# Kernel optimization log

Measured on AMD Instinct MI355X. Metric: run time of the kernel, lower is better.

## Reference

```python
import jax, jax.numpy as jnp
import numpy as np

B, S, H = 4, 2048, 1024
NH, HD = 8, 128  # num_heads, head_dim

def setup_inputs() -> dict:
    key = jax.random.key(0)
    ks = jax.random.split(key, 5)
    scale = 1.0 / np.sqrt(H)
    return {
        "hidden_states": jax.random.normal(ks[0], (B, S, H), dtype=jnp.float32),
        "Wq": jax.random.normal(ks[1], (H, H), dtype=jnp.float32) * scale,
        "Wk": jax.random.normal(ks[2], (H, H), dtype=jnp.float32) * scale,
        "Wv": jax.random.normal(ks[3], (H, H), dtype=jnp.float32) * scale,
        "Wo": jax.random.normal(ks[4], (H, H), dtype=jnp.float32) * scale,
    }

def reference(hidden_states, Wq, Wk, Wv, Wo):
    # projections (torch Linear: x @ W.T), weights stored [out, in]
    q = hidden_states @ Wq.T
    k = hidden_states @ Wk.T
    v = hidden_states @ Wv.T
    # [B, NH, S, HD]
    q = q.reshape(B, S, NH, HD).transpose(0, 2, 1, 3)
    k = k.reshape(B, S, NH, HD).transpose(0, 2, 1, 3)
    v = v.reshape(B, S, NH, HD).transpose(0, 2, 1, 3)
    scale = 1.0 / jnp.sqrt(jnp.asarray(HD, dtype=q.dtype))
    scores = jnp.einsum("bhqd,bhkd->bhqk", q, k) * scale
    # softmax in fp32, cast back to input dtype (matches torch F.softmax dtype=float32)
    attn = jax.nn.softmax(scores.astype(jnp.float32), axis=-1).astype(q.dtype)
    out = jnp.einsum("bhqk,bhkd->bhqd", attn, v)
    out = out.transpose(0, 2, 1, 3).reshape(B, S, H)
    return out @ Wo.T
```

## Files before the change

kernel.cpp:

```cpp
#include <hip/hip_runtime.h>
#include <stdint.h>

#define Bz  4
#define Sz  2048
#define Hz  1024
#define NHz 8
#define HDz 128
#define Mz  (Bz*Sz)

typedef __attribute__((ext_vector_type(8))) short bf16x8;
typedef __attribute__((ext_vector_type(4))) float f32x4;

__device__ __forceinline__ unsigned short f2bf(float x) {
  union { float f; unsigned int u; } c; c.f = x;
  unsigned int u = c.u;
  return (unsigned short)((u + 0x7FFFu + ((u >> 16) & 1u)) >> 16);
}

__device__ __forceinline__ void gl2lds16(const unsigned short* g, unsigned short* l) {
  __builtin_amdgcn_global_load_lds(
      (const __attribute__((address_space(1))) unsigned int*)g,
      (__attribute__((address_space(3))) unsigned int*)l, 16, 0, 0);
}

__global__ __launch_bounds__(256)
void cvt_kernel(const float* __restrict__ in, unsigned short* __restrict__ out, int n) {
  const int n4 = n >> 2;
  for (int i = blockIdx.x * blockDim.x + threadIdx.x; i < n4; i += gridDim.x * blockDim.x) {
    float4 v = ((const float4*)in)[i];
    ushort4 o;
    o.x = f2bf(v.x); o.y = f2bf(v.y); o.z = f2bf(v.z); o.w = f2bf(v.w);
    ((ushort4*)out)[i] = o;
  }
}

__global__ __launch_bounds__(256)
void cvt4_kernel(const float* __restrict__ w0, const float* __restrict__ w1,
                 const float* __restrict__ w2, const float* __restrict__ w3,
                 unsigned short* __restrict__ o0, unsigned short* __restrict__ o1,
                 unsigned short* __restrict__ o2, unsigned short* __restrict__ o3) {
  const int which = blockIdx.y;
  const float* in = (which == 0) ? w0 : (which == 1) ? w1 : (which == 2) ? w2 : w3;
  unsigned short* out = (which == 0) ? o0 : (which == 1) ? o1 : (which == 2) ? o2 : o3;
  const int n4 = (Hz * Hz) >> 2;
  for (int i = blockIdx.x * blockDim.x + threadIdx.x; i < n4; i += gridDim.x * blockDim.x) {
    float4 v = ((const float4*)in)[i];
    ushort4 o;
    o.x = f2bf(v.x); o.y = f2bf(v.y); o.z = f2bf(v.z); o.w = f2bf(v.w);
    ((ushort4*)out)[i] = o;
  }
}

#define GEMM_PROLOG()                                                           \
  __shared__ __align__(16) unsigned short Asm[128 * 64];                        \
  __shared__ __align__(16) unsigned short Bsm[128 * 64];                        \
  const int tid = threadIdx.x;                                                  \
  const int w  = tid >> 6, l = tid & 63;                                        \
  const int lc = l & 15,  lg = l >> 4;                                          \
  const int wr = w >> 1,  wc = w & 1;                                           \
  const int bm = blockIdx.x * 128;                                              \
  const int bn = blockIdx.y * 128;                                              \
  f32x4 acc[4][4];                                                              \
  _Pragma("unroll")                                                             \
  for (int i = 0; i < 4; i++)                                                   \
    _Pragma("unroll")                                                           \
    for (int j = 0; j < 4; j++) acc[i][j] = (f32x4){0.f, 0.f, 0.f, 0.f};        \
  const int srow = w * 32 + (l >> 3);                                           \
  const int scol = (l & 7) * 8;                                                 \
  for (int kt = 0; kt < 16; kt++) {                                             \
    const int k0 = kt * 64;                                                     \
    __syncthreads();                                                            \
    _Pragma("unroll")                                                           \
    for (int i = 0; i < 4; i++) {                                               \
      gl2lds16(A  + (size_t)(bm + srow + i * 8) * Hz + k0 + scol,               \
               &Asm[(w * 32 + i * 8) * 64]);                                    \
      gl2lds16(Bw + (size_t)(bn + srow + i * 8) * Hz + k0 + scol,               \
               &Bsm[(w * 32 + i * 8) * 64]);                                    \
    }                                                                           \
    __syncthreads();                                                            \
    _Pragma("unroll")                                                           \
    for (int kk = 0; kk < 2; kk++) {                                            \
      bf16x8 af[4], bf[4];                                                      \
      _Pragma("unroll")                                                         \
      for (int t = 0; t < 4; t++) {                                             \
        af[t] = *(const bf16x8*)&Asm[(wr*64 + t*16 + lc)*64 + kk*32 + lg*8];    \
        bf[t] = *(const bf16x8*)&Bsm[(wc*64 + t*16 + lc)*64 + kk*32 + lg*8];    \
      }                                                                         \
      _Pragma("unroll")                                                         \
      for (int mt = 0; mt < 4; mt++)                                            \
        _Pragma("unroll")                                                       \
        for (int nt = 0; nt < 4; nt++)                                          \
          acc[mt][nt] = __builtin_amdgcn_mfma_f32_16x16x32_bf16(                \
              af[mt], bf[nt], acc[mt][nt], 0, 0, 0);                            \
    }                                                                           \
  }

__global__ __launch_bounds__(256)
void gemm_qkv(const unsigned short* __restrict__ A,
              const unsigned short* __restrict__ W0,
              const unsigned short* __restrict__ W1,
              const unsigned short* __restrict__ W2,
              unsigned short* __restrict__ Qo,
              unsigned short* __restrict__ Ko,
              unsigned short* __restrict__ Vto, float qscale)
{
  const int z = blockIdx.z;
  const unsigned short* Bw = (z == 0) ? W0 : (z == 1) ? W1 : W2;
  const float alpha = (z == 0) ? qscale : 1.0f;
  GEMM_PROLOG()

#pragma unroll
  for (int mt = 0; mt < 4; mt++) {
#pragma unroll
    for (int nt = 0; nt < 4; nt++) {
      const int row0 = bm + wr * 64 + mt * 16 + lg * 4;
      const int col  = bn + wc * 64 + nt * 16 + lc;
      if (z == 2) {
        ushort4 pk;
        pk.x = f2bf(acc[mt][nt][0]);
        pk.y = f2bf(acc[mt][nt][1]);
        pk.z = f2bf(acc[mt][nt][2]);
        pk.w = f2bf(acc[mt][nt][3]);
        const size_t idx = ((size_t)((row0 >> 11) << 10) + col) * Sz + (row0 & 2047);
        *(ushort4*)&Vto[idx] = pk;
      } else {
        unsigned short* C = (z == 0) ? Qo : Ko;
#pragma unroll
        for (int r = 0; r < 4; r++)
          C[(size_t)(row0 + r) * Hz + col] = f2bf(acc[mt][nt][r] * alpha);
      }
    }
  }
}

__global__ __launch_bounds__(256)
void gemm_out(const unsigned short* __restrict__ A,
              const unsigned short* __restrict__ Bw,
              float* __restrict__ C)
{
  GEMM_PROLOG()
#pragma unroll
  for (int mt = 0; mt < 4; mt++)
#pragma unroll
    for (int nt = 0; nt < 4; nt++) {
      const int row0 = bm + wr * 64 + mt * 16 + lg * 4;
      const int col  = bn + wc * 64 + nt * 16 + lc;
#pragma unroll
      for (int r = 0; r < 4; r++)
        C[(size_t)(row0 + r) * Hz + col] = acc[mt][nt][r];
    }
}

__global__ __launch_bounds__(256, 2)
void attn_fwd(const unsigned short* __restrict__ Q,
              const unsigned short* __restrict__ K,
              const unsigned short* __restrict__ Vt,
              unsigned short* __restrict__ O)
{
  const int bid = blockIdx.x;
  const int wg  = (bid & 7) * 64 + (bid >> 3);
  const int qb  = wg & 15;
  const int bh  = wg >> 4;
  const int b = bh >> 3, nh = bh & 7;
  const int w = threadIdx.x >> 6, l = threadIdx.x & 63;
  const int lc = l & 15, lg = l >> 4;

  __shared__ __align__(16) unsigned short Ksm[2][64 * 128];
  __shared__ __align__(16) unsigned short Vsm[128 * 64];
  __shared__ __align__(16) unsigned short Psm[4][16 * 64];

  bf16x8 qf[2][4];
#pragma unroll
  for (int mt = 0; mt < 2; mt++)
#pragma unroll
    for (int ks = 0; ks < 4; ks++)
      qf[mt][ks] = *(const bf16x8*)(Q + ((size_t)b * Sz + qb * 128 + w * 32 + mt * 16 + lc) * Hz
                                      + nh * HDz + ks * 32 + lg * 8);

  const unsigned short* Kbase = K  + (size_t)b * Sz * Hz + nh * HDz;
  const unsigned short* Vbase = Vt + (size_t)bh * HDz * Sz;

  f32x4 acc[2][8];
#pragma unroll
  for (int mt = 0; mt < 2; mt++)
#pragma unroll
    for (int i = 0; i < 8; i++) acc[mt][i] = (f32x4){0.f, 0.f, 0.f, 0.f};
  float mrow[2][4], lrow[2][4];
#pragma unroll
  for (int mt = 0; mt < 2; mt++)
#pragma unroll
    for (int r = 0; r < 4; r++) { mrow[mt][r] = -1e30f; lrow[mt][r] = 0.f; }

  #define STAGE_K(BUF, KT) {                                                          \
    _Pragma("unroll")                                                                 \
    for (int i = 0; i < 4; i++) {                                                     \
      const int r = w * 16 + i * 4 + (l >> 4);                                        \
      gl2lds16(Kbase + (size_t)((KT) * 64 + r) * Hz + (((l & 15) ^ (r & 7)) * 8),     \
               &Ksm[BUF][(w * 16 + i * 4) * 128]);                                    \
    } }
  #define STAGE_V(KT) {                                                               \
    _Pragma("unroll")                                                                 \
    for (int i = 0; i < 4; i++) {                                                     \
      const int r = w * 32 + i * 8 + (l >> 3);                                        \
      gl2lds16(Vbase + (size_t)r * Sz + (KT) * 64 + (((l & 7) ^ (r & 7)) * 8),        \
               &Vsm[(w * 32 + i * 8) * 64]);                                          \
    } }

  int cur = 0;
  STAGE_K(0, 0);
  __syncthreads();

  for (int kt = 0; kt < Sz / 64; kt++) {
    STAGE_V(kt);
    if (kt < Sz / 64 - 1) STAGE_K(cur ^ 1, kt + 1);

    f32x4 s[2][4];
#pragma unroll
    for (int mt = 0; mt < 2; mt++)
#pragma unroll
      for (int nt = 0; nt < 4; nt++) s[mt][nt] = (f32x4){0.f, 0.f, 0.f, 0.f};
#pragma unroll
    for (int ks = 0; ks < 4; ks++) {
#pragma unroll
      for (int nt = 0; nt < 4; nt++) {
        bf16x8 kf = *(const bf16x8*)&Ksm[cur][(nt * 16 + lc) * 128 + (((ks * 4 + lg) ^ (lc & 7)) * 8)];
#pragma unroll
        for (int mt = 0; mt < 2; mt++)
          s[mt][nt] = __builtin_amdgcn_mfma_f32_16x16x32_bf16(qf[mt][ks], kf, s[mt][nt], 0, 0, 0);
      }
    }

#pragma unroll
    for (int mt = 0; mt < 2; mt++) {
#pragma unroll
      for (int r = 0; r < 4; r++) {
        float tm = fmaxf(fmaxf(s[mt][0][r], s[mt][1][r]), fmaxf(s[mt][2][r], s[mt][3][r]));
        tm = fmaxf(tm, __shfl_xor(tm, 1));
        tm = fmaxf(tm, __shfl_xor(tm, 2));
        tm = fmaxf(tm, __shfl_xor(tm, 4));
        tm = fmaxf(tm, __shfl_xor(tm, 8));
        if (tm > mrow[mt][r] + 8.0f) {
          const float sc = exp2f(mrow[mt][r] - tm);
          mrow[mt][r] = tm;
          lrow[mt][r] *= sc;
#pragma unroll
          for (int nt = 0; nt < 8; nt++) acc[mt][nt][r] *= sc;
        }
        float rs = 0.f;
#pragma unroll
        for (int nt = 0; nt < 4; nt++) {
          float p = exp2f(s[mt][nt][r] - mrow[mt][r]);
          s[mt][nt][r] = p;
          rs += p;
        }
        lrow[mt][r] += rs;
      }
    }

    bf16x8 pf[2][2];
#pragma unroll
    for (int mt = 0; mt < 2; mt++) {
#pragma unroll
      for (int nt = 0; nt < 4; nt++)
#pragma unroll
        for (int r = 0; r < 4; r++) {
          const int row = lg * 4 + r;
          const int ch  = (nt * 2 + (lc >> 3)) ^ (row & 7);
          Psm[w][row * 64 + ch * 8 + (lc & 7)] = f2bf(s[mt][nt][r]);
        }
#pragma unroll
      for (int kk = 0; kk < 2; kk++)
        pf[mt][kk] = *(const bf16x8*)&Psm[w][lc * 64 + (((kk * 4 + lg) ^ (lc & 7)) * 8)];
    }

    __syncthreads();

#pragma unroll
    for (int kk = 0; kk < 2; kk++) {
#pragma unroll
      for (int nt = 0; nt < 8; nt++) {
        bf16x8 vf = *(const bf16x8*)&Vsm[(nt * 16 + lc) * 64 + (((kk * 4 + lg) ^ (lc & 7)) * 8)];
        acc[0][nt] = __builtin_amdgcn_mfma_f32_16x16x32_bf16(pf[0][kk], vf, acc[0][nt], 0, 0, 0);
        acc[1][nt] = __builtin_amdgcn_mfma_f32_16x16x32_bf16(pf[1][kk], vf, acc[1][nt], 0, 0, 0);
      }
    }

    __syncthreads();
    cur ^= 1;
  }

#pragma unroll
  for (int mt = 0; mt < 2; mt++) {
    float inv[4];
#pragma unroll
    for (int r = 0; r < 4; r++) {
      float t = lrow[mt][r];
      t += __shfl_xor(t, 1);
      t += __shfl_xor(t, 2);
      t += __shfl_xor(t, 4);
      t += __shfl_xor(t, 8);
      inv[r] = 1.0f / t;
    }
#pragma unroll
    for (int nt = 0; nt < 8; nt++)
#pragma unroll
      for (int r = 0; r < 4; r++) {
        const size_t row = (size_t)b * Sz + qb * 128 + w * 32 + mt * 16 + lg * 4 + r;
        O[row * Hz + nh * HDz + nt * 16 + lc] = f2bf(acc[mt][nt][r] * inv[r]);
      }
  }
}

extern "C" void kernel_launch(void* const* d_in, const int* in_sizes, int n_in,
                              void* d_out, int out_size, void* d_ws, size_t ws_size,
                              hipStream_t stream) {
  const float* hs = (const float*)d_in[0];
  const float* Wq = (const float*)d_in[1];
  const float* Wk = (const float*)d_in[2];
  const float* Wv = (const float*)d_in[3];
  const float* Wo = (const float*)d_in[4];

  const size_t NEL = (size_t)Mz * Hz;
  const size_t WEL = (size_t)Hz * Hz;

  unsigned short* p = (unsigned short*)d_ws;
  unsigned short* hs_bf = p; p += NEL;
  unsigned short* Wq_bf = p; p += WEL;
  unsigned short* Wk_bf = p; p += WEL;
  unsigned short* Wv_bf = p; p += WEL;
  unsigned short* Wo_bf = p; p += WEL;
  unsigned short* Qb    = p; p += NEL;
  unsigned short* Kb    = p; p += NEL;
  unsigned short* Vtb   = p; p += NEL;
  unsigned short* Ob    = hs_bf;

  cvt_kernel<<<2048, 256, 0, stream>>>(hs, hs_bf, (int)NEL);
  cvt4_kernel<<<dim3(512, 4), 256, 0, stream>>>(Wq, Wk, Wv, Wo,
                                                Wq_bf, Wk_bf, Wv_bf, Wo_bf);

  const float qscale = 0.08838834764831845f * 1.44269504088896340736f;
  gemm_qkv<<<dim3(Mz / 128, Hz / 128, 3), 256, 0, stream>>>(
      hs_bf, Wq_bf, Wk_bf, Wv_bf, Qb, Kb, Vtb, qscale);

  attn_fwd<<<512, 256, 0, stream>>>(Qb, Kb, Vtb, Ob);

  gemm_out<<<dim3(Mz / 128, Hz / 128), 256, 0, stream>>>(Ob, Wo_bf, (float*)d_out);
}
```

Before: 339.5 us.

## Switch attention to 32x32 MFMA with transposed S and register-resident P

Rewrites the attention kernel's inner loop to use 32x32x16 bf16 MFMA and computes S transposed (K as the A operand), so each lane holds one query row's scores. Row max and sum need only a single cross-half shuffle, and P is packed with v_cvt_pk_bf16_f32 and rearranged through lane shuffles instead of a round trip through shared memory. The goal is to cut LDS traffic, shuffle count and the P staging buffer. The cost is extra per-element shuffles when the running max is rescaled, at the output, and in the P lane exchange.

```diff
diff --git a/kernel.cpp b/kernel.cpp
--- a/kernel.cpp
+++ b/kernel.cpp
@@ -10,11 +10,18 @@
 
 typedef __attribute__((ext_vector_type(8))) short bf16x8;
 typedef __attribute__((ext_vector_type(4))) float f32x4;
+typedef __attribute__((ext_vector_type(16))) float f32x16;
 
 __device__ __forceinline__ unsigned short f2bf(float x) {
   union { float f; unsigned int u; } c; c.f = x;
   unsigned int u = c.u;
   return (unsigned short)((u + 0x7FFFu + ((u >> 16) & 1u)) >> 16);
+}
+
+__device__ __forceinline__ unsigned cvtpk(float lo, float hi_) {
+  unsigned r;
+  asm("v_cvt_pk_bf16_f32 %0, %1, %2" : "=v"(r) : "v"(lo), "v"(hi_));
+  return r;
 }
 
 __device__ __forceinline__ void gl2lds16(const unsigned short* g, unsigned short* l) {
@@ -163,33 +170,28 @@
   const int bh  = wg >> 4;
   const int b = bh >> 3, nh = bh & 7;
   const int w = threadIdx.x >> 6, l = threadIdx.x & 63;
-  const int lc = l & 15, lg = l >> 4;
+  const int l31 = l & 31, hi = l >> 5;
 
   __shared__ __align__(16) unsigned short Ksm[2][64 * 128];
   __shared__ __align__(16) unsigned short Vsm[128 * 64];
-  __shared__ __align__(16) unsigned short Psm[4][16 * 64];
-
-  bf16x8 qf[2][4];
-#pragma unroll
-  for (int mt = 0; mt < 2; mt++)
-#pragma unroll
-    for (int ks = 0; ks < 4; ks++)
-      qf[mt][ks] = *(const bf16x8*)(Q + ((size_t)b * Sz + qb * 128 + w * 32 + mt * 16 + lc) * Hz
-                                      + nh * HDz + ks * 32 + lg * 8);
+
+  bf16x8 qf[8];
+#pragma unroll
+  for (int ks = 0; ks < 8; ks++)
+    qf[ks] = *(const bf16x8*)(Q + ((size_t)b * Sz + qb * 128 + w * 32 + l31) * Hz
+                                + nh * HDz + ks * 16 + hi * 8);
 
   const unsigned short* Kbase = K  + (size_t)b * Sz * Hz + nh * HDz;
   const unsigned short* Vbase = Vt + (size_t)bh * HDz * Sz;
 
-  f32x4 acc[2][8];
-#pragma unroll
-  for (int mt = 0; mt < 2; mt++)
-#pragma unroll
-    for (int i = 0; i < 8; i++) acc[mt][i] = (f32x4){0.f, 0.f, 0.f, 0.f};
-  float mrow[2][4], lrow[2][4];
-#pragma unroll
-  for (int mt = 0; mt < 2; mt++)
-#pragma unroll
-    for (int r = 0; r < 4; r++) { mrow[mt][r] = -1e30f; lrow[mt][r] = 0.f; }
+  f32x16 acc[4];
+#pragma unroll
+  for (int d = 0; d < 4; d++)
+#pragma unroll
+    for (int i = 0; i < 16; i++) acc[d][i] = 0.f;
+  float mrow = -3.0e38f, lrowp = 0.f;
+
+  union PA { unsigned wd[4]; bf16x8 v; };
 
   #define STAGE_K(BUF, KT) {                                                          \
     _Pragma("unroll")                                                                 \
@@ -214,100 +216,96 @@
     STAGE_V(kt);
     if (kt < Sz / 64 - 1) STAGE_K(cur ^ 1, kt + 1);
 
-    f32x4 s[2][4];
-#pragma unroll
-    for (int mt = 0; mt < 2; mt++)
-#pragma unroll
-      for (int nt = 0; nt < 4; nt++) s[mt][nt] = (f32x4){0.f, 0.f, 0.f, 0.f};
-#pragma unroll
-    for (int ks = 0; ks < 4; ks++) {
-#pragma unroll
-      for (int nt = 0; nt < 4; nt++) {
-        bf16x8 kf = *(const bf16x8*)&Ksm[cur][(nt * 16 + lc) * 128 + (((ks * 4 + lg) ^ (lc & 7)) * 8)];
-#pragma unroll
-        for (int mt = 0; mt < 2; mt++)
-          s[mt][nt] = __builtin_amdgcn_mfma_f32_16x16x32_bf16(qf[mt][ks], kf, s[mt][nt], 0, 0, 0);
-      }
-    }
-
-#pragma unroll
-    for (int mt = 0; mt < 2; mt++) {
-#pragma unroll
-      for (int r = 0; r < 4; r++) {
-        float tm = fmaxf(fmaxf(s[mt][0][r], s[mt][1][r]), fmaxf(s[mt][2][r], s[mt][3][r]));
-        tm = fmaxf(tm, __shfl_xor(tm, 1));
-        tm = fmaxf(tm, __shfl_xor(tm, 2));
-        tm = fmaxf(tm, __shfl_xor(tm, 4));
-        tm = fmaxf(tm, __shfl_xor(tm, 8));
-        if (tm > mrow[mt][r] + 8.0f) {
-          const float sc = exp2f(mrow[mt][r] - tm);
-          mrow[mt][r] = tm;
-          lrow[mt][r] *= sc;
-#pragma unroll
-          for (int nt = 0; nt < 8; nt++) acc[mt][nt][r] *= sc;
+    f32x16 st[2];
+#pragma unroll
+    for (int i = 0; i < 16; i++) { st[0][i] = 0.f; st[1][i] = 0.f; }
+#pragma unroll
+    for (int ks = 0; ks < 8; ks++) {
+      bf16x8 kf0 = *(const bf16x8*)&Ksm[cur][(l31) * 128 + (((ks * 2 + hi) ^ (l31 & 7)) * 8)];
+      st[0] = __builtin_amdgcn_mfma_f32_32x32x16_bf16(kf0, qf[ks], st[0], 0, 0, 0);
+      bf16x8 kf1 = *(const bf16x8*)&Ksm[cur][(32 + l31) * 128 + (((ks * 2 + hi) ^ (l31 & 7)) * 8)];
+      st[1] = __builtin_amdgcn_mfma_f32_32x32x16_bf16(kf1, qf[ks], st[1], 0, 0, 0);
+    }
+
+    float t16[16];
+#pragma unroll
+    for (int i = 0; i < 16; i++) t16[i] = fmaxf(st[0][i], st[1][i]);
+#pragma unroll
+    for (int s = 8; s > 0; s >>= 1)
+#pragma unroll
+      for (int i = 0; i < s; i++) t16[i] = fmaxf(t16[i], t16[i + s]);
+    const float tm = fmaxf(t16[0], __shfl_xor(t16[0], 32));
+
+    float sc = 1.0f;
+    const bool trig = tm > mrow + 8.0f;
+    if (trig) { sc = exp2f(mrow - tm); mrow = tm; lrowp *= sc; }
+    if (__any(trig)) {
+#pragma unroll
+      for (int r = 0; r < 16; r++) {
+        const float scr = __shfl(sc, (r & 3) + 8 * (r >> 2) + 4 * hi);
+#pragma unroll
+        for (int d = 0; d < 4; d++) acc[d][r] *= scr;
+      }
+    }
+
+    float ps = 0.f;
+#pragma unroll
+    for (int n = 0; n < 2; n++)
+#pragma unroll
+      for (int i = 0; i < 16; i++) {
+        const float p = exp2f(st[n][i] - mrow);
+        st[n][i] = p;
+        ps += p;
+      }
+    lrowp += ps;
+
+    PA pa[4];
+#pragma unroll
+    for (int n = 0; n < 2; n++) {
+      unsigned Wp[8];
+#pragma unroll
+      for (int m = 0; m < 4; m++) {
+        Wp[m * 2 + 0] = cvtpk(st[n][4 * m + 0], st[n][4 * m + 1]);
+        Wp[m * 2 + 1] = cvtpk(st[n][4 * m + 2], st[n][4 * m + 3]);
+      }
+#pragma unroll
+      for (int ks2 = 0; ks2 < 2; ks2++) {
+#pragma unroll
+        for (int h = 0; h < 2; h++) {
+          const unsigned a0 = Wp[(2 * ks2) * 2 + h];
+          const unsigned a1 = Wp[(2 * ks2 + 1) * 2 + h];
+          const unsigned own  = hi ? a1 : a0;
+          const unsigned send = hi ? a0 : a1;
+          const unsigned part = __shfl_xor(send, 32);
+          pa[n * 2 + ks2].wd[0 + h] = hi ? part : own;
+          pa[n * 2 + ks2].wd[2 + h] = hi ? own : part;
         }
-        float rs = 0.f;
-#pragma unroll
-        for (int nt = 0; nt < 4; nt++) {
-          float p = exp2f(s[mt][nt][r] - mrow[mt][r]);
-          s[mt][nt][r] = p;
-          rs += p;
-        }
-        lrow[mt][r] += rs;
-      }
-    }
-
-    bf16x8 pf[2][2];
-#pragma unroll
-    for (int mt = 0; mt < 2; mt++) {
-#pragma unroll
-      for (int nt = 0; nt < 4; nt++)
-#pragma unroll
-        for (int r = 0; r < 4; r++) {
-          const int row = lg * 4 + r;
-          const int ch  = (nt * 2 + (lc >> 3)) ^ (row & 7);
-          Psm[w][row * 64 + ch * 8 + (lc & 7)] = f2bf(s[mt][nt][r]);
-        }
-#pragma unroll
-      for (int kk = 0; kk < 2; kk++)
-        pf[mt][kk] = *(const bf16x8*)&Psm[w][lc * 64 + (((kk * 4 + lg) ^ (lc & 7)) * 8)];
+      }
     }
 
     __syncthreads();
 
 #pragma unroll
-    for (int kk = 0; kk < 2; kk++) {
-#pragma unroll
-      for (int nt = 0; nt < 8; nt++) {
-        bf16x8 vf = *(const bf16x8*)&Vsm[(nt * 16 + lc) * 64 + (((kk * 4 + lg) ^ (lc & 7)) * 8)];
-        acc[0][nt] = __builtin_amdgcn_mfma_f32_16x16x32_bf16(pf[0][kk], vf, acc[0][nt], 0, 0, 0);
-        acc[1][nt] = __builtin_amdgcn_mfma_f32_16x16x32_bf16(pf[1][kk], vf, acc[1][nt], 0, 0, 0);
-      }
-    }
+    for (int t = 0; t < 4; t++)
+#pragma unroll
+      for (int d = 0; d < 4; d++) {
+        bf16x8 vf = *(const bf16x8*)&Vsm[(d * 32 + l31) * 64 + (((t * 2 + hi) ^ (l31 & 7)) * 8)];
+        acc[d] = __builtin_amdgcn_mfma_f32_32x32x16_bf16(pa[t].v, vf, acc[d], 0, 0, 0);
+      }
 
     __syncthreads();
     cur ^= 1;
   }
 
-#pragma unroll
-  for (int mt = 0; mt < 2; mt++) {
-    float inv[4];
-#pragma unroll
-    for (int r = 0; r < 4; r++) {
-      float t = lrow[mt][r];
-      t += __shfl_xor(t, 1);
-      t += __shfl_xor(t, 2);
-      t += __shfl_xor(t, 4);
-      t += __shfl_xor(t, 8);
-      inv[r] = 1.0f / t;
-    }
-#pragma unroll
-    for (int nt = 0; nt < 8; nt++)
-#pragma unroll
-      for (int r = 0; r < 4; r++) {
-        const size_t row = (size_t)b * Sz + qb * 128 + w * 32 + mt * 16 + lg * 4 + r;
-        O[row * Hz + nh * HDz + nt * 16 + lc] = f2bf(acc[mt][nt][r] * inv[r]);
-      }
+  const float lsum = lrowp + __shfl_xor(lrowp, 32);
+  const float inv = 1.0f / lsum;
+#pragma unroll
+  for (int r = 0; r < 16; r++) {
+    const float ir = __shfl(inv, (r & 3) + 8 * (r >> 2) + 4 * hi);
+    const size_t row = (size_t)b * Sz + qb * 128 + w * 32 + (r & 3) + 8 * (r >> 2) + 4 * hi;
+#pragma unroll
+    for (int d = 0; d < 4; d++)
+      O[row * Hz + nh * HDz + d * 32 + l31] = f2bf(acc[d][r] * ir);
   }
 }
 
```

Result: faster. 295.8 us (-12.9%).
